# Optimization experiments

Measured on AMD Instinct MI355X. Metric: run time of the kernel, lower is better.

Reference implementation:

```python
import jax, jax.numpy as jnp
import numpy as np

DIM = 1024
HEADS = 16
DIM_HEAD = 64
INNER = HEADS * DIM_HEAD  # 1024
MLP = 4096
NQ = 16384
NW = 1024
LN_EPS = 1e-5
L2_EPS = 1e-12


def setup_inputs() -> dict:
    key = jax.random.key(0)
    ks = jax.random.split(key, 12)
    s = 0.02
    return {
        "queries": jax.random.normal(ks[0], (NQ, DIM), jnp.float32),
        "prototypes": jax.random.normal(ks[1], (NW, DIM), jnp.float32),
        "ln1_w": 1.0 + s * jax.random.normal(ks[2], (DIM,), jnp.float32),
        "ln1_b": s * jax.random.normal(ks[3], (DIM,), jnp.float32),
        "wq": s * jax.random.normal(ks[4], (DIM, INNER), jnp.float32),
        "wk": s * jax.random.normal(ks[5], (DIM, INNER), jnp.float32),
        "wv": s * jax.random.normal(ks[6], (DIM, INNER), jnp.float32),
        "wo": s * jax.random.normal(ks[7], (INNER, DIM), jnp.float32),
        "bo": jnp.zeros((DIM,), jnp.float32),
        "ln2_w": 1.0 + s * jax.random.normal(ks[8], (DIM,), jnp.float32),
        "ln2_b": s * jax.random.normal(ks[9], (DIM,), jnp.float32),
        "w1": s * jax.random.normal(ks[10], (DIM, MLP), jnp.float32),
        "b1": jnp.zeros((MLP,), jnp.float32),
        "w2": s * jax.random.normal(ks[11], (MLP, DIM), jnp.float32),
        "b2": jnp.zeros((DIM,), jnp.float32),
    }


def _layernorm(x, w, b):
    mu = jnp.mean(x, axis=-1, keepdims=True)
    var = jnp.mean(jnp.square(x - mu), axis=-1, keepdims=True)
    return (x - mu) * jax.lax.rsqrt(var + LN_EPS) * w + b


def _l2norm(x):
    n = jnp.sqrt(jnp.sum(jnp.square(x), axis=-1, keepdims=True))
    return x / jnp.maximum(n, L2_EPS)


def reference(queries, prototypes, ln1_w, ln1_b, wq, wk, wv, wo, bo,
              ln2_w, ln2_b, w1, b1, w2, b2):
    residual = queries
    qn = _layernorm(queries, ln1_w, ln1_b)
    pn = _layernorm(prototypes, ln1_w, ln1_b)
    # projections -> (h, q, d) / (h, n, d)
    q = (qn @ wq).reshape(NQ, HEADS, DIM_HEAD).transpose(1, 0, 2)
    k = (pn @ wk).reshape(NW, HEADS, DIM_HEAD).transpose(1, 0, 2)
    v = (pn @ wv).reshape(NW, HEADS, DIM_HEAD).transpose(1, 0, 2)
    attn = jnp.einsum('hqd,hnd->hqn', _l2norm(q), _l2norm(k))  # cosine, no softmax
    out = jnp.einsum('hqn,hnd->hqd', attn, v)
    out = out.transpose(1, 0, 2).reshape(NQ, INNER)
    out = out @ wo + bo + residual
    residual2 = out
    h = _layernorm(out, ln2_w, ln2_b)
    h = jax.nn.gelu(h @ w1 + b1, approximate=False) @ w2 + b2
    return h + residual2
```

## Files before the change

### kernel.cpp

```cpp
#include <hip/hip_runtime.h>
#include <hip/hip_bf16.h>

typedef _Float16 f16;
typedef __attribute__((ext_vector_type(8))) _Float16 f16x8;
typedef __attribute__((ext_vector_type(4))) _Float16 f16x4;
typedef __attribute__((ext_vector_type(4))) float f32x4;

#define DIM 1024
#define HEADS 16
#define DHEAD 64
#define MLPD 4096
#define NQ 16384
#define NW 1024
#define MCHUNK 32

#define WAITV(n) asm volatile("s_waitcnt vmcnt(" #n ")" ::: "memory")
#define WAITL0 asm volatile("s_waitcnt lgkmcnt(0)" ::: "memory")

__device__ __forceinline__ void glds16(const f16* g, f16* l) {
  __builtin_amdgcn_global_load_lds(
      (const __attribute__((address_space(1))) void*)g,
      (__attribute__((address_space(3))) void*)l, 16, 0, 0);
}

__global__ __launch_bounds__(256) void ln_f16_k(
    const float* __restrict__ X, const float* __restrict__ w,
    const float* __restrict__ b, f16* __restrict__ O) {
  const int row = blockIdx.x;
  const int t = threadIdx.x;
  const float4 v = ((const float4*)(X + (long)row * DIM))[t];
  float s = v.x + v.y + v.z + v.w;
  float s2 = v.x * v.x + v.y * v.y + v.z * v.z + v.w * v.w;
#pragma unroll
  for (int m = 1; m < 64; m <<= 1) {
    s += __shfl_xor(s, m);
    s2 += __shfl_xor(s2, m);
  }
  __shared__ float ps[4], ps2[4];
  const int lane = t & 63, wid = t >> 6;
  if (lane == 0) { ps[wid] = s; ps2[wid] = s2; }
  __syncthreads();
  s = ps[0] + ps[1] + ps[2] + ps[3];
  s2 = ps2[0] + ps2[1] + ps2[2] + ps2[3];
  const float mu = s * (1.0f / DIM);
  const float inv = rsqrtf(s2 * (1.0f / DIM) - mu * mu + 1e-5f);
  const float4 wv = ((const float4*)w)[t];
  const float4 bv = ((const float4*)b)[t];
  f16x4 o;
  o[0] = (f16)((v.x - mu) * inv * wv.x + bv.x);
  o[1] = (f16)((v.y - mu) * inv * wv.y + bv.y);
  o[2] = (f16)((v.z - mu) * inv * wv.z + bv.z);
  o[3] = (f16)((v.w - mu) * inv * wv.w + bv.w);
  *(f16x4*)(O + (long)row * DIM + t * 4) = o;
}

__global__ __launch_bounds__(256) void tcast_k(const float* __restrict__ X,
                                               f16* __restrict__ O, int R, int C) {
  __shared__ float tile[32][33];
  const int c0 = blockIdx.x * 32, r0 = blockIdx.y * 32;
  const int tx = threadIdx.x, ty = threadIdx.y;
#pragma unroll
  for (int j = 0; j < 4; ++j)
    tile[ty + j * 8][tx] = X[(long)(r0 + ty + j * 8) * C + c0 + tx];
  __syncthreads();
#pragma unroll
  for (int j = 0; j < 4; ++j)
    O[(long)(c0 + ty + j * 8) * R + r0 + tx] = (f16)tile[tx][ty + j * 8];
}

__global__ __launch_bounds__(256) void calc_m_part_k(const f16* __restrict__ kh,
                                                     const f16* __restrict__ v,
                                                     float* __restrict__ Mp) {
  const int h = blockIdx.x, ch = blockIdx.y;
  const int t = threadIdx.x;
  const int d1 = t >> 2;
  const int d2b = (t & 3) * 16;
  float acc[16] = {};
  const int n0 = ch * (NW / MCHUNK);
#pragma unroll 4
  for (int n = n0; n < n0 + NW / MCHUNK; ++n) {
    const float kv = (float)kh[(long)n * DIM + h * DHEAD + d1];
    const f16x8* vp = (const f16x8*)&v[(long)n * DIM + h * DHEAD + d2b];
    const f16x8 v0 = vp[0], v1 = vp[1];
#pragma unroll
    for (int j = 0; j < 8; ++j) acc[j] += kv * (float)v0[j];
#pragma unroll
    for (int j = 0; j < 8; ++j) acc[8 + j] += kv * (float)v1[j];
  }
  float* o = &Mp[((long)(h * MCHUNK + ch)) * 4096 + d1 * 64 + d2b];
#pragma unroll
  for (int j = 0; j < 16; ++j) o[j] = acc[j];
}

__global__ __launch_bounds__(256) void calc_m_reduce_k(const float* __restrict__ Mp,
                                                       float* __restrict__ Mo) {
  const int h = blockIdx.x;
  const int t = threadIdx.x;
#pragma unroll
  for (int e = t; e < 4096; e += 256) {
    float s = 0.f;
#pragma unroll
    for (int c = 0; c < MCHUNK; ++c)
      s += Mp[((long)(h * MCHUNK + c)) * 4096 + e];
    Mo[h * 4096 + e] = s;
  }
}

__global__ __launch_bounds__(256) void calc_wefft_k(const float* __restrict__ M,
                                                    const float* __restrict__ wo,
                                                    f16* __restrict__ Wt) {
  const int h = blockIdx.x, jt = blockIdx.y;
  const int t = threadIdx.x;
  const int jl = t & 63;
  const int il0 = (t >> 6) * 16;
  const int j = jt * 64 + jl;
  float acc[16] = {};
  for (int d = 0; d < DHEAD; ++d) {
    const float w = wo[(long)(h * DHEAD + d) * DIM + j];
    const float* mrow = &M[h * 4096 + il0 * 64 + d];
#pragma unroll
    for (int r = 0; r < 16; ++r) acc[r] += mrow[r * 64] * w;
  }
#pragma unroll
  for (int r = 0; r < 16; ++r)
    Wt[(long)j * DIM + h * DHEAD + il0 + r] = (f16)acc[r];
}

enum {
  EPI_F16 = 0,
  EPI_L2N = 1,
  EPI_BIAS_RES = 2,
  EPI_GELU = 3
};

template <int EPI>
__global__ __launch_bounds__(512, 2) void gemm256(
    const f16* __restrict__ A, const f16* __restrict__ Bt, int M, int N, int K,
    const float* __restrict__ bias, const float* resid, void* out) {
  __shared__ __align__(16) f16 lds[65536];

  const int tid = threadIdx.x;
  const int lane = tid & 63;
  const int wid = tid >> 6;
  const int wm = wid >> 2;
  const int wn = wid & 3;
  const int l15 = lane & 15;

  int bm, bn;
  {
    const int orig = blockIdx.y * gridDim.x + blockIdx.x;
    if ((gridDim.x & 7) == 0) {
      const int slab = orig & 7;
      const int idx = orig >> 3;
      const int sm = gridDim.x >> 3;
      bm = slab * sm + idx % sm;
      bn = idx / sm;
    } else {
      bm = blockIdx.x;
      bn = blockIdx.y;
    }
  }

  const int scol8 = (((tid & 3) ^ ((tid >> 3) & 3))) * 8;
  const f16* aSrc = A + (long)(bm * 256 + (tid >> 2)) * K + scol8;
  const f16* bSrc = Bt + (long)(bn * 256 + (tid >> 2)) * K + scol8;
  const long hK = (long)128 * K;
  const int tid8 = tid * 8;

  const int rslot8 = (((lane >> 4) ^ ((l15 >> 1) & 3))) * 8;
  const int aRdBase = (wm * 128 + l15) * 32 + rslot8;
  const int bRdBase = 16384 + (wn * 64 + l15) * 32 + rslot8;

  f32x4 acc[8][4] = {};
  const int NT = K >> 6;

  glds16(aSrc, &lds[tid8]);
  glds16(aSrc + hK, &lds[4096 + tid8]);
  glds16(bSrc, &lds[16384 + tid8]);
  glds16(bSrc + hK, &lds[16384 + 4096 + tid8]);
  glds16(aSrc + 32, &lds[8192 + tid8]);
  glds16(aSrc + hK + 32, &lds[8192 + 4096 + tid8]);
  glds16(bSrc + 32, &lds[24576 + tid8]);
  glds16(bSrc + hK + 32, &lds[24576 + 4096 + tid8]);
  glds16(aSrc + 64, &lds[32768 + tid8]);
  glds16(aSrc + hK + 64, &lds[32768 + 4096 + tid8]);
  glds16(bSrc + 64, &lds[32768 + 16384 + tid8]);
  glds16(bSrc + hK + 64, &lds[32768 + 16384 + 4096 + tid8]);
  WAITV(8);
  __builtin_amdgcn_s_barrier();

#define PHASE_CORE(KS, MH, LOADB)                                        \
  {                                                                      \
    const f16* Ap = L + (KS)*8192 + aRdBase + (MH)*2048;                 \
    a[0] = *(const f16x8*)(Ap);                                          \
    a[1] = *(const f16x8*)(Ap + 512);                                    \
    a[2] = *(const f16x8*)(Ap + 1024);                                   \
    a[3] = *(const f16x8*)(Ap + 1536);                                   \
    if (LOADB) {                                                         \
      const f16* Bp = L + (KS)*8192 + bRdBase;                           \
      b[0] = *(const f16x8*)(Bp);                                        \
      b[1] = *(const f16x8*)(Bp + 512);                                  \
      b[2] = *(const f16x8*)(Bp + 1024);                                 \
      b[3] = *(const f16x8*)(Bp + 1536);                                 \
    }                                                                    \
    __builtin_amdgcn_s_barrier();                                        \
    WAITL0;                                                              \
    __builtin_amdgcn_sched_barrier(0);                                   \
    __builtin_amdgcn_s_setprio(1);                                       \
    _Pragma("unroll") for (int j = 0; j < 4; ++j)                        \
        _Pragma("unroll") for (int nj = 0; nj < 4; ++nj)                 \
            acc[(MH)*4 + j][nj] = __builtin_amdgcn_mfma_f32_16x16x32_f16(\
                a[j], b[nj], acc[(MH)*4 + j][nj], 0, 0, 0);              \
    __builtin_amdgcn_s_setprio(0);                                       \
  }

  for (int g = 0; g < NT; ++g) {
    f16* L = &lds[(g & 1) * 32768];
    f16* Lo = &lds[((g & 1) ^ 1) * 32768];
    const long ko1 = (long)(g + 1) * 64;
    const long ko2 = (long)(g + 2) * 64;
    const bool s1 = (g + 1) < NT, s2 = (g + 2) < NT;
    f16x8 a[4], b[4];

    if (s1) {
      glds16(aSrc + ko1 + 32, Lo + 8192 + tid8);
      glds16(aSrc + hK + ko1 + 32, Lo + 8192 + 4096 + tid8);
    }
    PHASE_CORE(0, 0, 1);
    __builtin_amdgcn_s_barrier();

    if (s1) {
      glds16(bSrc + ko1 + 32, Lo + 24576 + tid8);
      glds16(bSrc + hK + ko1 + 32, Lo + 24576 + 4096 + tid8);
    }
    PHASE_CORE(0, 1, 0);
    if (s1) { WAITV(8); } else { WAITV(0); }
    __builtin_amdgcn_s_barrier();

    if (s2) {
      glds16(aSrc + ko2, L + tid8);
      glds16(aSrc + hK + ko2, L + 4096 + tid8);
    }
    PHASE_CORE(1, 0, 1);
    __builtin_amdgcn_s_barrier();

    if (s2) {
      glds16(bSrc + ko2, L + 16384 + tid8);
      glds16(bSrc + hK + ko2, L + 16384 + 4096 + tid8);
    }
    PHASE_CORE(1, 1, 0);
    if (s2) { WAITV(8); } else if (s1) { WAITV(4); }
    __builtin_amdgcn_s_barrier();
  }
#undef PHASE_CORE

  const int r0 = bm * 256 + wm * 128;
  const int c0 = bn * 256 + wn * 64;
  const int lr = (lane >> 4) * 4;
  const int lc = l15;

#pragma unroll
  for (int mi = 0; mi < 8; ++mi) {
#pragma unroll
    for (int i = 0; i < 4; ++i) {
      const long r = r0 + mi * 16 + lr + i;
      if (EPI == EPI_L2N) {
        float ss = 0.f;
#pragma unroll
        for (int nj = 0; nj < 4; ++nj) {
          const float x = acc[mi][nj][i];
          ss += x * x;
        }
        ss += __shfl_xor(ss, 1);
        ss += __shfl_xor(ss, 2);
        ss += __shfl_xor(ss, 4);
        ss += __shfl_xor(ss, 8);
        const float inv = 1.0f / fmaxf(sqrtf(ss), 1e-12f);
#pragma unroll
        for (int nj = 0; nj < 4; ++nj)
          ((f16*)out)[r * N + c0 + nj * 16 + lc] = (f16)(acc[mi][nj][i] * inv);
      } else if (EPI == EPI_F16) {
#pragma unroll
        for (int nj = 0; nj < 4; ++nj)
          ((f16*)out)[r * N + c0 + nj * 16 + lc] = (f16)acc[mi][nj][i];
      } else if (EPI == EPI_BIAS_RES) {
#pragma unroll
        for (int nj = 0; nj < 4; ++nj) {
          const long c = c0 + nj * 16 + lc;
          ((float*)out)[r * N + c] = acc[mi][nj][i] + bias[c] + resid[r * N + c];
        }
      } else {
#pragma unroll
        for (int nj = 0; nj < 4; ++nj) {
          const long c = c0 + nj * 16 + lc;
          const float x = acc[mi][nj][i] + bias[c];
          const float u = 0.7978845608028654f * (x + 0.044715f * x * x * x);
          const float z = __expf(fminf(-2.0f * u, 88.0f));
          const float th = (1.0f - z) / (1.0f + z);
          ((f16*)out)[r * N + c] = (f16)(0.5f * x * (1.0f + th));
        }
      }
    }
  }
}

extern "C" void kernel_launch(void* const* d_in, const int* in_sizes, int n_in,
                              void* d_out, int out_size, void* d_ws, size_t ws_size,
                              hipStream_t stream) {
  (void)in_sizes; (void)n_in; (void)out_size;
  const float* queries = (const float*)d_in[0];
  const float* prototypes = (const float*)d_in[1];
  const float* ln1_w = (const float*)d_in[2];
  const float* ln1_b = (const float*)d_in[3];
  const float* wq = (const float*)d_in[4];
  const float* wk = (const float*)d_in[5];
  const float* wv = (const float*)d_in[6];
  const float* wo = (const float*)d_in[7];
  const float* bo = (const float*)d_in[8];
  const float* ln2_w = (const float*)d_in[9];
  const float* ln2_b = (const float*)d_in[10];
  const float* w1 = (const float*)d_in[11];
  const float* b1 = (const float*)d_in[12];
  const float* w2 = (const float*)d_in[13];
  const float* b2 = (const float*)d_in[14];

  char* ws = (char*)d_ws;
  const size_t MB = 1024ull * 1024ull;
  if (ws_size < 176ull * MB) return;

  f16* QN = (f16*)(ws + 0);
  f16* QHAT = (f16*)(ws + 32 * MB);
  f16* PN = (f16*)(ws + 64 * MB);
  f16* WQT = (f16*)(ws + 66 * MB);
  f16* WKT = (f16*)(ws + 68 * MB);
  f16* WVT = (f16*)(ws + 70 * MB);
  f16* KHAT = (f16*)(ws + 72 * MB);
  f16* VBF = (f16*)(ws + 74 * MB);
  float* Mbuf = (float*)(ws + 76 * MB);
  f16* WEFFT = (f16*)(ws + 77 * MB);
  float* Mpart = (float*)(ws + 0);
  f16* G = (f16*)(ws + 0);
  f16* HBF = (f16*)(ws + 128 * MB);
  f16* W1T = (f16*)(ws + 160 * MB);
  f16* W2T = (f16*)(ws + 168 * MB);
  float* RES2 = (float*)d_out;

  ln_f16_k<<<NQ, 256, 0, stream>>>(queries, ln1_w, ln1_b, QN);
  ln_f16_k<<<NW, 256, 0, stream>>>(prototypes, ln1_w, ln1_b, PN);
  tcast_k<<<dim3(32, 32), dim3(32, 8), 0, stream>>>(wq, WQT, DIM, DIM);
  tcast_k<<<dim3(32, 32), dim3(32, 8), 0, stream>>>(wk, WKT, DIM, DIM);
  tcast_k<<<dim3(32, 32), dim3(32, 8), 0, stream>>>(wv, WVT, DIM, DIM);
  tcast_k<<<dim3(128, 32), dim3(32, 8), 0, stream>>>(w1, W1T, DIM, MLPD);
  tcast_k<<<dim3(32, 128), dim3(32, 8), 0, stream>>>(w2, W2T, MLPD, DIM);

  gemm256<EPI_L2N><<<dim3(NQ / 256, DIM / 256), 512, 0, stream>>>(
      QN, WQT, NQ, DIM, DIM, nullptr, nullptr, QHAT);
  gemm256<EPI_L2N><<<dim3(NW / 256, DIM / 256), 512, 0, stream>>>(
      PN, WKT, NW, DIM, DIM, nullptr, nullptr, KHAT);
  gemm256<EPI_F16><<<dim3(NW / 256, DIM / 256), 512, 0, stream>>>(
      PN, WVT, NW, DIM, DIM, nullptr, nullptr, VBF);

  calc_m_part_k<<<dim3(HEADS, MCHUNK), 256, 0, stream>>>(KHAT, VBF, Mpart);
  calc_m_reduce_k<<<HEADS, 256, 0, stream>>>(Mpart, Mbuf);
  calc_wefft_k<<<dim3(HEADS, 16), 256, 0, stream>>>(Mbuf, wo, WEFFT);

  gemm256<EPI_BIAS_RES><<<dim3(NQ / 256, DIM / 256), 512, 0, stream>>>(
      QHAT, WEFFT, NQ, DIM, DIM, bo, queries, RES2);

  ln_f16_k<<<NQ, 256, 0, stream>>>(RES2, ln2_w, ln2_b, HBF);

  gemm256<EPI_GELU><<<dim3(NQ / 256, MLPD / 256), 512, 0, stream>>>(
      HBF, W1T, NQ, MLPD, DIM, b1, nullptr, G);
  gemm256<EPI_BIAS_RES><<<dim3(NQ / 256, DIM / 256), 512, 0, stream>>>(
      G, W2T, NQ, DIM, MLPD, b2, RES2, (float*)d_out);
}
```

Measured before the change: 655.7 us.

## Restructure GEMM main loop to register double-buffered fragments with one barrier per tile

Replaces the four-phase, half-tile staggered global-to-LDS pipeline (with explicit vmcnt waits and a barrier per phase) with a simpler whole-tile double buffer and a single __syncthreads per K-iteration. LDS fragment reads for the next MFMA burst are issued ahead of the current burst, and the first fragments of the next tile are prefetched into registers after the barrier. The aim is to cut barrier and wait overhead and to overlap LDS reads with MFMAs. In exchange, prefetch depth drops from two tiles ahead to one, which may expose global load latency, and the extra fragment registers raise register pressure.

```diff
diff --git a/kernel.cpp b/kernel.cpp
--- a/kernel.cpp
+++ b/kernel.cpp
@@ -13,9 +13,6 @@
 #define NQ 16384
 #define NW 1024
 #define MCHUNK 32
-
-#define WAITV(n) asm volatile("s_waitcnt vmcnt(" #n ")" ::: "memory")
-#define WAITL0 asm volatile("s_waitcnt lgkmcnt(0)" ::: "memory")
 
 __device__ __forceinline__ void glds16(const f16* g, f16* l) {
   __builtin_amdgcn_global_load_lds(
@@ -174,85 +171,77 @@
   f32x4 acc[8][4] = {};
   const int NT = K >> 6;
 
-  glds16(aSrc, &lds[tid8]);
-  glds16(aSrc + hK, &lds[4096 + tid8]);
-  glds16(bSrc, &lds[16384 + tid8]);
-  glds16(bSrc + hK, &lds[16384 + 4096 + tid8]);
-  glds16(aSrc + 32, &lds[8192 + tid8]);
-  glds16(aSrc + hK + 32, &lds[8192 + 4096 + tid8]);
-  glds16(bSrc + 32, &lds[24576 + tid8]);
-  glds16(bSrc + hK + 32, &lds[24576 + 4096 + tid8]);
-  glds16(aSrc + 64, &lds[32768 + tid8]);
-  glds16(aSrc + hK + 64, &lds[32768 + 4096 + tid8]);
-  glds16(bSrc + 64, &lds[32768 + 16384 + tid8]);
-  glds16(bSrc + hK + 64, &lds[32768 + 16384 + 4096 + tid8]);
-  WAITV(8);
-  __builtin_amdgcn_s_barrier();
-
-#define PHASE_CORE(KS, MH, LOADB)                                        \
-  {                                                                      \
-    const f16* Ap = L + (KS)*8192 + aRdBase + (MH)*2048;                 \
-    a[0] = *(const f16x8*)(Ap);                                          \
-    a[1] = *(const f16x8*)(Ap + 512);                                    \
-    a[2] = *(const f16x8*)(Ap + 1024);                                   \
-    a[3] = *(const f16x8*)(Ap + 1536);                                   \
-    if (LOADB) {                                                         \
-      const f16* Bp = L + (KS)*8192 + bRdBase;                           \
-      b[0] = *(const f16x8*)(Bp);                                        \
-      b[1] = *(const f16x8*)(Bp + 512);                                  \
-      b[2] = *(const f16x8*)(Bp + 1024);                                 \
-      b[3] = *(const f16x8*)(Bp + 1536);                                 \
-    }                                                                    \
-    __builtin_amdgcn_s_barrier();                                        \
-    WAITL0;                                                              \
-    __builtin_amdgcn_sched_barrier(0);                                   \
-    __builtin_amdgcn_s_setprio(1);                                       \
-    _Pragma("unroll") for (int j = 0; j < 4; ++j)                        \
-        _Pragma("unroll") for (int nj = 0; nj < 4; ++nj)                 \
-            acc[(MH)*4 + j][nj] = __builtin_amdgcn_mfma_f32_16x16x32_f16(\
-                a[j], b[nj], acc[(MH)*4 + j][nj], 0, 0, 0);              \
-    __builtin_amdgcn_s_setprio(0);                                       \
-  }
+#define STAGE_A0(Ld, ko)                              \
+  glds16(aSrc + (ko), (Ld) + tid8);                   \
+  glds16(aSrc + hK + (ko), (Ld) + 4096 + tid8)
+#define STAGE_A1(Ld, ko)                              \
+  glds16(aSrc + (ko) + 32, (Ld) + 8192 + tid8);       \
+  glds16(aSrc + hK + (ko) + 32, (Ld) + 8192 + 4096 + tid8)
+#define STAGE_B0(Ld, ko)                              \
+  glds16(bSrc + (ko), (Ld) + 16384 + tid8);           \
+  glds16(bSrc + hK + (ko), (Ld) + 16384 + 4096 + tid8)
+#define STAGE_B1(Ld, ko)                              \
+  glds16(bSrc + (ko) + 32, (Ld) + 24576 + tid8);      \
+  glds16(bSrc + hK + (ko) + 32, (Ld) + 24576 + 4096 + tid8)
+
+#define BURST(AF, BF, MB)                                                 \
+  __builtin_amdgcn_s_setprio(1);                                          \
+  _Pragma("unroll") for (int j = 0; j < 4; ++j)                           \
+      _Pragma("unroll") for (int nj = 0; nj < 4; ++nj)                    \
+          acc[(MB) + j][nj] = __builtin_amdgcn_mfma_f32_16x16x32_f16(     \
+              AF[j], BF[nj], acc[(MB) + j][nj], 0, 0, 0);                 \
+  __builtin_amdgcn_s_setprio(0)
+
+  STAGE_A0(lds, 0);
+  STAGE_B0(lds, 0);
+  STAGE_A1(lds, 0);
+  STAGE_B1(lds, 0);
+  __syncthreads();
+
+  f16x8 bA[4], bB[4], aA[4], aB[4], aC[4], aD[4];
+#pragma unroll
+  for (int j = 0; j < 4; ++j) bA[j] = *(const f16x8*)&lds[bRdBase + j * 512];
+#pragma unroll
+  for (int j = 0; j < 4; ++j) aA[j] = *(const f16x8*)&lds[aRdBase + j * 512];
 
   for (int g = 0; g < NT; ++g) {
     f16* L = &lds[(g & 1) * 32768];
     f16* Lo = &lds[((g & 1) ^ 1) * 32768];
     const long ko1 = (long)(g + 1) * 64;
-    const long ko2 = (long)(g + 2) * 64;
-    const bool s1 = (g + 1) < NT, s2 = (g + 2) < NT;
-    f16x8 a[4], b[4];
-
+    const bool s1 = (g + 1) < NT;
+
+    if (s1) { STAGE_A0(Lo, ko1); STAGE_B0(Lo, ko1); }
+#pragma unroll
+    for (int j = 0; j < 4; ++j)
+      aB[j] = *(const f16x8*)&L[aRdBase + 2048 + j * 512];
+    BURST(aA, bA, 0);
+    if (s1) { STAGE_A1(Lo, ko1); STAGE_B1(Lo, ko1); }
+#pragma unroll
+    for (int j = 0; j < 4; ++j)
+      bB[j] = *(const f16x8*)&L[8192 + bRdBase + j * 512];
+#pragma unroll
+    for (int j = 0; j < 4; ++j)
+      aC[j] = *(const f16x8*)&L[8192 + aRdBase + j * 512];
+    BURST(aB, bA, 4);
+#pragma unroll
+    for (int j = 0; j < 4; ++j)
+      aD[j] = *(const f16x8*)&L[8192 + aRdBase + 2048 + j * 512];
+    BURST(aC, bB, 0);
+    BURST(aD, bB, 4);
+
+    __syncthreads();
     if (s1) {
-      glds16(aSrc + ko1 + 32, Lo + 8192 + tid8);
-      glds16(aSrc + hK + ko1 + 32, Lo + 8192 + 4096 + tid8);
+#pragma unroll
+      for (int j = 0; j < 4; ++j) bA[j] = *(const f16x8*)&Lo[bRdBase + j * 512];
+#pragma unroll
+      for (int j = 0; j < 4; ++j) aA[j] = *(const f16x8*)&Lo[aRdBase + j * 512];
     }
-    PHASE_CORE(0, 0, 1);
-    __builtin_amdgcn_s_barrier();
-
-    if (s1) {
-      glds16(bSrc + ko1 + 32, Lo + 24576 + tid8);
-      glds16(bSrc + hK + ko1 + 32, Lo + 24576 + 4096 + tid8);
-    }
-    PHASE_CORE(0, 1, 0);
-    if (s1) { WAITV(8); } else { WAITV(0); }
-    __builtin_amdgcn_s_barrier();
-
-    if (s2) {
-      glds16(aSrc + ko2, L + tid8);
-      glds16(aSrc + hK + ko2, L + 4096 + tid8);
-    }
-    PHASE_CORE(1, 0, 1);
-    __builtin_amdgcn_s_barrier();
-
-    if (s2) {
-      glds16(bSrc + ko2, L + 16384 + tid8);
-      glds16(bSrc + hK + ko2, L + 16384 + 4096 + tid8);
-    }
-    PHASE_CORE(1, 1, 0);
-    if (s2) { WAITV(8); } else if (s1) { WAITV(4); }
-    __builtin_amdgcn_s_barrier();
-  }
-#undef PHASE_CORE
+  }
+#undef STAGE_A0
+#undef STAGE_A1
+#undef STAGE_B0
+#undef STAGE_B1
+#undef BURST
 
   const int r0 = bm * 256 + wm * 128;
   const int c0 = bn * 256 + wn * 64;
```

Result: faster. 636.4 us (-2.9%).
